# Kernel optimization log

Hardware: AMD Instinct MI355X
Metric: run time of the kernel (lower is better)

Reference implementation:

```python
import jax, jax.numpy as jnp
import numpy as np

N_ATOMS = 4096
N_EDGES = 131072
NUM_ELEMENTS = 100
NUM_BESSEL = 8
CUTOFF = 6.0
D_NODE = 64
D_MSG = 128
SH_DIM = 9            # l=0,1,2 -> 1+3+5
TP_IN = D_MSG * SH_DIM  # 1152
N_HEADS = 4
HEAD_DIM = D_MSG // N_HEADS


def setup_inputs() -> dict:
    key = jax.random.key(0)
    ks = jax.random.split(key, 20)
    def p(k, shape):
        return jax.random.normal(k, shape, dtype=jnp.float32) * 0.05
    z = lambda n: jnp.zeros((n,), jnp.float32)
    return {
        "atomic_numbers": jax.random.randint(ks[0], (N_ATOMS,), 0, NUM_ELEMENTS),
        "positions": jax.random.normal(ks[1], (N_ATOMS, 3), dtype=jnp.float32),
        "edge_index": jax.random.randint(ks[2], (2, N_EDGES), 0, N_ATOMS),
        "edge_vectors": jax.random.normal(ks[3], (N_EDGES, 3), dtype=jnp.float32),
        "edge_lengths": jax.random.uniform(ks[4], (N_EDGES,), dtype=jnp.float32, minval=0.5, maxval=5.5),
        "embed_table": p(ks[5], (NUM_ELEMENTS, D_NODE)),
        "W_r1": p(ks[6], (NUM_BESSEL, 64)), "b_r1": z(64),
        "W_r2": p(ks[7], (64, D_MSG)), "b_r2": z(D_MSG),
        "W_tp": p(ks[8], (TP_IN, D_MSG)), "b_tp": z(D_MSG),
        "W_m1": p(ks[9], (D_MSG, D_MSG)), "b_m1": z(D_MSG),
        "W_m2": p(ks[10], (D_MSG, D_MSG)), "b_m2": z(D_MSG),
        "W_qkv": p(ks[11], (D_MSG, 3 * D_MSG)), "b_qkv": z(3 * D_MSG),
        "W_ao": p(ks[12], (D_MSG, D_MSG)), "b_ao": z(D_MSG),
        "W_g": p(ks[13], (D_MSG, D_MSG)), "b_g": z(D_MSG),
        "W_o": p(ks[14], (D_MSG, D_MSG)), "b_o": z(D_MSG),
    }


def reference(atomic_numbers, positions, edge_index, edge_vectors, edge_lengths,
              embed_table, W_r1, b_r1, W_r2, b_r2, W_tp, b_tp,
              W_m1, b_m1, W_m2, b_m2, W_qkv, b_qkv, W_ao, b_ao,
              W_g, b_g, W_o, b_o):
    node_features = embed_table[atomic_numbers]  # [N, 64]

    # spherical harmonics (l = 0,1,2 -> 9 features), order as in source
    r = jnp.linalg.norm(edge_vectors, axis=-1, keepdims=True) + 1e-8
    u = edge_vectors / r
    x, y, z = u[:, 0], u[:, 1], u[:, 2]
    sh = jnp.stack([jnp.ones_like(x), y, z, x,
                    3.0 * z * z - 1.0, x * z, y * z, x * y, x * x - y * y], axis=-1)  # [E,9]

    # bessel RBF with cosine cutoff envelope
    freqs = jnp.arange(1, NUM_BESSEL + 1, dtype=jnp.float32) * (np.pi / CUTOFF)
    env = 0.5 * (jnp.cos(edge_lengths * (np.pi / CUTOFF)) + 1.0) * (edge_lengths < CUTOFF).astype(jnp.float32)
    rbf = jnp.sin(edge_lengths[:, None] * freqs) / edge_lengths[:, None] * env[:, None]  # [E,8]

    radial = jax.nn.silu(rbf @ W_r1 + b_r1)
    radial = jax.nn.silu(radial @ W_r2 + b_r2)  # [E,128]

    # per-edge outer product radial x sh, flattened per-l blocks then concatenated
    outer = radial[:, :, None] * sh[:, None, :]  # [E,128,9]
    E = outer.shape[0]
    edge_messages = jnp.concatenate([
        outer[:, :, 0:1].reshape(E, -1),   # l=0 -> 128
        outer[:, :, 1:4].reshape(E, -1),   # l=1 -> 384
        outer[:, :, 4:9].reshape(E, -1),   # l=2 -> 640
    ], axis=-1)                            # [E,1152]
    edge_messages = edge_messages @ W_tp + b_tp  # [E,128]

    # scatter-add aggregation onto destination nodes (index_add_)
    dst = edge_index[1]
    aggregated = jnp.zeros((node_features.shape[0], D_MSG), jnp.float32).at[dst].add(edge_messages)

    combined = jnp.concatenate([node_features, aggregated[:, :D_NODE]], axis=-1)  # [N,128]
    updated = jax.nn.silu(combined @ W_m1 + b_m1) @ W_m2 + b_m2                   # [N,128]

    # multi-head self-attention over all atoms (batch=1, seq=N)
    N = updated.shape[0]
    qkv = updated @ W_qkv + b_qkv
    q, k, v = jnp.split(qkv, 3, axis=-1)
    q = q.reshape(N, N_HEADS, HEAD_DIM)
    k = k.reshape(N, N_HEADS, HEAD_DIM)
    v = v.reshape(N, N_HEADS, HEAD_DIM)
    scores = jnp.einsum('nhd,mhd->hnm', q, k) / np.sqrt(HEAD_DIM).astype(np.float32)
    attn = jax.nn.softmax(scores, axis=-1)
    attended = jnp.einsum('hnm,mhd->nhd', attn, v).reshape(N, D_MSG)
    attended = attended @ W_ao + b_ao

    gate = jax.nn.sigmoid(updated @ W_g + b_g)
    out = gate * attended + (1.0 - gate) * updated
    return out @ W_o + b_o
```

## Files before the change

### kernel.cpp

```cpp
#include <hip/hip_runtime.h>
#include <hip/hip_bf16.h>
#include <math.h>

#define N_ATOMS 4096
#define N_EDGES 131072
#define PI6 0.52359877559829887308f

typedef __attribute__((ext_vector_type(4))) float f32x4;
typedef _Float16 h16;
typedef __attribute__((ext_vector_type(8))) _Float16 half8;

__device__ __forceinline__ float silu_f(float x) { return x / (1.0f + __expf(-x)); }

__device__ __forceinline__ unsigned pk2h(float lo, float hi) {
    h16 a = (h16)lo, b = (h16)hi;
    unsigned short ua, ub;
    __builtin_memcpy(&ua, &a, 2);
    __builtin_memcpy(&ub, &b, 2);
    return ((unsigned)ub << 16) | (unsigned)ua;
}

__global__ void wprep_kernel(const float* __restrict__ Wtp, float* __restrict__ Wsl)
{
    int idx = blockIdx.x * 256 + threadIdx.x;
    int o = idx & 63;
    int c = (idx >> 6) & 127;
    int s = idx >> 13;
    int row = (s == 0) ? c : (s < 4 ? 128 + c * 3 + (s - 1) : 512 + c * 5 + (s - 4));
    Wsl[idx] = Wtp[row * 128 + o];
}

__global__ void count_kernel(const int* __restrict__ eidx, int* __restrict__ deg)
{
    int e = blockIdx.x * 256 + threadIdx.x;
    atomicAdd(&deg[eidx[N_EDGES + e]], 1);
}

__global__ void scan_kernel(const int* __restrict__ deg, int* __restrict__ base,
                            int* __restrict__ cur)
{
    __shared__ int sums[1024];
    const int t = threadIdx.x;
    int v0 = deg[4*t], v1 = deg[4*t+1], v2 = deg[4*t+2], v3 = deg[4*t+3];
    int s = v0 + v1 + v2 + v3;
    sums[t] = s;
    __syncthreads();
    for (int off = 1; off < 1024; off <<= 1) {
        int x = (t >= off) ? sums[t - off] : 0;
        __syncthreads();
        sums[t] += x;
        __syncthreads();
    }
    int excl = (t > 0) ? sums[t - 1] : 0;
    base[4*t]   = excl;             cur[4*t]   = excl;
    base[4*t+1] = excl + v0;        cur[4*t+1] = excl + v0;
    base[4*t+2] = excl + v0 + v1;   cur[4*t+2] = excl + v0 + v1;
    base[4*t+3] = excl + v0 + v1 + v2; cur[4*t+3] = excl + v0 + v1 + v2;
}

__global__ void scatter_kernel(const int* __restrict__ eidx, int* __restrict__ cur,
                               int* __restrict__ sortedE)
{
    int e = blockIdx.x * 256 + threadIdx.x;
    int dst = eidx[N_EDGES + e];
    int p = atomicAdd(&cur[dst], 1);
    sortedE[p] = e;
}

__global__ __launch_bounds__(128) void agg_kernel(
    const float* __restrict__ evec, const float* __restrict__ elen,
    const int* __restrict__ sortedE, const int* __restrict__ base,
    const int* __restrict__ deg,
    const float* __restrict__ Wr1, const float* __restrict__ br1,
    const float* __restrict__ Wr2, const float* __restrict__ br2,
    const float* __restrict__ Wsl, const float* __restrict__ btp,
    float* __restrict__ agg)
{
    __shared__ float rbfL[4][8];
    __shared__ float shL[4][9];
    __shared__ __align__(16) float R1L[4][64];
    __shared__ __align__(16) float GL[1152];
    __shared__ __align__(16) float redL[8][64];

    const int t = threadIdx.x;
    const int dst = blockIdx.x;
    const int dg = deg[dst];
    const int bs = base[dst];

    float G[9] = {0.f,0.f,0.f,0.f,0.f,0.f,0.f,0.f,0.f};

    const int nch = (dg + 3) >> 2;
    for (int c = 0; c < nch; ++c) {
        __syncthreads();
        if (t < 32) {
            int el = t >> 3, f = t & 7;
            int ce = c * 4 + el;
            float v = 0.f;
            if (ce < dg) {
                int eid = sortedE[bs + ce];
                float len = elen[eid];
                float env = 0.5f * (cosf(len * PI6) + 1.0f) * (len < 6.0f ? 1.0f : 0.0f);
                v = sinf(len * ((float)(f + 1) * PI6)) * (env / len);
            }
            rbfL[el][f] = v;
        } else if (t < 36) {
            int el = t - 32;
            int ce = c * 4 + el;
            float s0=0,s1=0,s2=0,s3=0,s4=0,s5=0,s6=0,s7=0,s8=0;
            if (ce < dg) {
                int eid = sortedE[bs + ce];
                float vx = evec[eid*3], vy = evec[eid*3+1], vz = evec[eid*3+2];
                float r = sqrtf(vx*vx + vy*vy + vz*vz) + 1e-8f;
                float inv = 1.0f / r;
                float x = vx*inv, y = vy*inv, z = vz*inv;
                s0 = 1.0f; s1 = y; s2 = z; s3 = x;
                s4 = 3.0f*z*z - 1.0f; s5 = x*z; s6 = y*z; s7 = x*y; s8 = x*x - y*y;
            }
            shL[el][0]=s0; shL[el][1]=s1; shL[el][2]=s2; shL[el][3]=s3;
            shL[el][4]=s4; shL[el][5]=s5; shL[el][6]=s6; shL[el][7]=s7; shL[el][8]=s8;
        }
        __syncthreads();
        #pragma unroll
        for (int rep = 0; rep < 2; ++rep) {
            int tau = t + rep * 128;
            int el = tau >> 6, ko = tau & 63;
            float acc = br1[ko];
            #pragma unroll
            for (int f = 0; f < 8; ++f)
                acc = fmaf(rbfL[el][f], Wr1[f * 64 + ko], acc);
            R1L[el][ko] = silu_f(acc);
        }
        __syncthreads();
        float a0 = 0.f, a1 = 0.f, a2 = 0.f, a3 = 0.f;
        for (int j = 0; j < 64; ++j) {
            float w = Wr2[j * 128 + t];
            a0 = fmaf(R1L[0][j], w, a0);
            a1 = fmaf(R1L[1][j], w, a1);
            a2 = fmaf(R1L[2][j], w, a2);
            a3 = fmaf(R1L[3][j], w, a3);
        }
        float b2 = br2[t];
        int rem = dg - c * 4;
        if (rem > 0) { float r2 = silu_f(a0 + b2);
            #pragma unroll
            for (int s2 = 0; s2 < 9; ++s2) G[s2] = fmaf(shL[0][s2], r2, G[s2]); }
        if (rem > 1) { float r2 = silu_f(a1 + b2);
            #pragma unroll
            for (int s2 = 0; s2 < 9; ++s2) G[s2] = fmaf(shL[1][s2], r2, G[s2]); }
        if (rem > 2) { float r2 = silu_f(a2 + b2);
            #pragma unroll
            for (int s2 = 0; s2 < 9; ++s2) G[s2] = fmaf(shL[2][s2], r2, G[s2]); }
        if (rem > 3) { float r2 = silu_f(a3 + b2);
            #pragma unroll
            for (int s2 = 0; s2 < 9; ++s2) G[s2] = fmaf(shL[3][s2], r2, G[s2]); }
    }

    #pragma unroll
    for (int s2 = 0; s2 < 9; ++s2) GL[s2 * 128 + t] = G[s2];
    __syncthreads();

    const f32x4* Wsl4 = (const f32x4*)Wsl;
    const int og = (t & 15) * 4;
    const int q  = t >> 4;
    f32x4 acc4 = {0.f, 0.f, 0.f, 0.f};
    for (int i = 0; i < 144; ++i) {
        int f = q * 144 + i;
        float g = GL[f];
        f32x4 w = Wsl4[f * 16 + (t & 15)];
        acc4 = acc4 + w * g;
    }
    *(f32x4*)&redL[q][og] = acc4;
    __syncthreads();
    if (t < 64) {
        float sum = 0.f;
        #pragma unroll
        for (int q2 = 0; q2 < 8; ++q2) sum += redL[q2][t];
        agg[dst * 64 + t] = sum + (float)dg * btp[t];
    }
}

__global__ void combined_kernel(const int* __restrict__ an,
                                const float* __restrict__ emb,
                                const float* __restrict__ agg,
                                float* __restrict__ comb)
{
    int i = blockIdx.x * 256 + threadIdx.x;
    if (i < N_ATOMS * 64) {
        int n = i >> 6, d = i & 63;
        comb[n * 128 + d]      = emb[an[n] * 64 + d];
        comb[n * 128 + 64 + d] = agg[n * 64 + d];
    }
}

template <int ACT>
__global__ __launch_bounds__(256, 2) void gemm128(
    const float* __restrict__ A, const float* __restrict__ W,
    const float* __restrict__ bias, float* __restrict__ C, int N,
    const float* __restrict__ aux1, const float* __restrict__ aux2)
{
    __shared__ __align__(16) float AT[128][64];
    __shared__ __align__(16) float Ws[128][64];
    const int t  = threadIdx.x;
    const int M0 = blockIdx.x * 64;
    const int N0 = blockIdx.y * 64;

    for (int idx = t; idx < 64 * 128; idx += 256) {
        int m = idx >> 7, k = idx & 127;
        AT[k][m ^ ((k & 15) << 2)] = A[(M0 + m) * 128 + k];
    }
    for (int idx = t; idx < 128 * 64; idx += 256) {
        int k = idx >> 6, o = idx & 63;
        Ws[k][o] = W[k * N + N0 + o];
    }
    __syncthreads();

    const int m0 = (t & 15) * 4;
    const int o0 = (t >> 4) * 4;
    float acc[4][4] = {};
    #pragma unroll 2
    for (int k = 0; k < 128; ++k) {
        int xs = (k & 15) << 2;
        float4 a4 = *(const float4*)&AT[k][m0 ^ xs];
        float4 w4 = *(const float4*)&Ws[k][o0];
        float av[4] = {a4.x, a4.y, a4.z, a4.w};
        float wv[4] = {w4.x, w4.y, w4.z, w4.w};
        #pragma unroll
        for (int i = 0; i < 4; ++i)
            #pragma unroll
            for (int j = 0; j < 4; ++j)
                acc[i][j] = fmaf(av[i], wv[j], acc[i][j]);
    }

    #pragma unroll
    for (int i = 0; i < 4; ++i) {
        int m = M0 + m0 + i;
        #pragma unroll
        for (int j = 0; j < 4; ++j) {
            int o = N0 + o0 + j;
            float v = acc[i][j] + bias[o];
            if (ACT == 1) v = silu_f(v);
            if (ACT == 2) {
                float sg = 1.0f / (1.0f + __expf(-v));
                v = sg * aux1[m * 128 + o] + (1.0f - sg) * aux2[m * 128 + o];
            }
            C[m * N + o] = v;
        }
    }
}

__global__ void qkprep_kernel(const float* __restrict__ qkvf,
                              h16* __restrict__ Qh, h16* __restrict__ Kh)
{
    int i = blockIdx.x * 256 + threadIdx.x;
    int d = i & 31, n = (i >> 5) & 4095, h = i >> 17;
    Qh[(h * 4096 + n) * 32 + d] = (h16)(qkvf[n * 384 + h * 32 + d] * 0.17677669529663687f);
    Kh[(h * 4096 + n) * 32 + d] = (h16)(qkvf[n * 384 + 128 + h * 32 + d]);
}

__global__ void vtprep_kernel(const float* __restrict__ qkvf,
                              h16* __restrict__ VT)
{
    int i = blockIdx.x * 256 + threadIdx.x;
    int n = i & 4095, dh = i >> 12;
    VT[dh * 4096 + n] = (h16)qkvf[n * 384 + 256 + dh];
}

__global__ __launch_bounds__(256, 4) void attn_kernel(
    const h16* __restrict__ Qh, const h16* __restrict__ Kh,
    const h16* __restrict__ VT, float* __restrict__ attd)
{
    __shared__ float st[4][64][10];
    const int t = threadIdx.x, w = t >> 6, lane = t & 63;
    const int h = blockIdx.x >> 8, qt = blockIdx.x & 255;
    const int l15 = lane & 15, g = lane >> 4;

    const h16* Kb = Kh + (size_t)h * 4096 * 32;
    const h16* Vb = VT + (size_t)h * 32 * 4096;
    half8 Qf = *(const half8*)(Qh + ((size_t)(h * 4096 + qt * 16 + l15) * 32 + g * 8));

    float m = -1e30f, l = 0.0f;
    f32x4 O0 = {0.f,0.f,0.f,0.f}, O1 = {0.f,0.f,0.f,0.f};
    const f32x4 zf = {0.f,0.f,0.f,0.f};
    const int sAlane = l15 + ((g & 1) << 5);
    const bool hi = g >= 2;

    const int kvbase = w * 1024;
    for (int kt = 0; kt < 32; ++kt) {
        int kv0 = kvbase + kt * 32;
        half8 K0 = *(const half8*)(Kb + ((size_t)(kv0 + l15) * 32 + g * 8));
        half8 K1 = *(const half8*)(Kb + ((size_t)(kv0 + 16 + l15) * 32 + g * 8));
        f32x4 S0 = __builtin_amdgcn_mfma_f32_16x16x32_f16(K0, Qf, zf, 0, 0, 0);
        f32x4 S1 = __builtin_amdgcn_mfma_f32_16x16x32_f16(K1, Qf, zf, 0, 0, 0);

        float tmax = fmaxf(fmaxf(fmaxf(S0.x, S0.y), fmaxf(S0.z, S0.w)),
                           fmaxf(fmaxf(S1.x, S1.y), fmaxf(S1.z, S1.w)));
        tmax = fmaxf(tmax, __shfl_xor(tmax, 16));
        tmax = fmaxf(tmax, __shfl_xor(tmax, 32));
        float mn = fmaxf(m, tmax);
        float c = __expf(m - mn);
        m = mn;
        float p0[4], p1[4];
        float ts = 0.f;
        #pragma unroll
        for (int i = 0; i < 4; ++i) { p0[i] = __expf(S0[i] - mn); ts += p0[i]; }
        #pragma unroll
        for (int i = 0; i < 4; ++i) { p1[i] = __expf(S1[i] - mn); ts += p1[i]; }
        ts += __shfl_xor(ts, 16);
        ts += __shfl_xor(ts, 32);
        l = l * c + ts;
        #pragma unroll
        for (int i = 0; i < 4; ++i) { O0[i] *= c; O1[i] *= c; }

        unsigned A0 = pk2h(p0[0], p0[1]), A1 = pk2h(p0[2], p0[3]);
        unsigned A2 = pk2h(p1[0], p1[1]), A3 = pk2h(p1[2], p1[3]);
        unsigned t0 = (unsigned)__shfl((int)A0, sAlane);
        unsigned t1 = (unsigned)__shfl((int)A1, sAlane);
        unsigned t2 = (unsigned)__shfl((int)A2, sAlane);
        unsigned t3 = (unsigned)__shfl((int)A3, sAlane);
        unsigned u0 = (unsigned)__shfl((int)A0, sAlane + 16);
        unsigned u1 = (unsigned)__shfl((int)A1, sAlane + 16);
        unsigned u2 = (unsigned)__shfl((int)A2, sAlane + 16);
        unsigned u3 = (unsigned)__shfl((int)A3, sAlane + 16);
        union { unsigned u[4]; half8 v; } P;
        P.u[0] = hi ? t2 : t0;
        P.u[1] = hi ? t3 : t1;
        P.u[2] = hi ? u2 : u0;
        P.u[3] = hi ? u3 : u1;

        half8 V0 = *(const half8*)(Vb + ((size_t)l15 * 4096 + kv0 + g * 8));
        half8 V1 = *(const half8*)(Vb + ((size_t)(16 + l15) * 4096 + kv0 + g * 8));
        O0 = __builtin_amdgcn_mfma_f32_16x16x32_f16(V0, P.v, O0, 0, 0, 0);
        O1 = __builtin_amdgcn_mfma_f32_16x16x32_f16(V1, P.v, O1, 0, 0, 0);
    }

    #pragma unroll
    for (int i = 0; i < 4; ++i) { st[w][lane][i] = O0[i]; st[w][lane][4 + i] = O1[i]; }
    st[w][lane][8] = m;
    st[w][lane][9] = l;
    __syncthreads();

    if (w == 0) {
        float M = -1e30f;
        #pragma unroll
        for (int j = 0; j < 4; ++j) M = fmaxf(M, st[j][lane][8]);
        float L = 0.f, o0[4] = {}, o1[4] = {};
        #pragma unroll
        for (int j = 0; j < 4; ++j) {
            float f = __expf(st[j][lane][8] - M);
            L += st[j][lane][9] * f;
            #pragma unroll
            for (int i = 0; i < 4; ++i) {
                o0[i] = fmaf(st[j][lane][i], f, o0[i]);
                o1[i] = fmaf(st[j][lane][4 + i], f, o1[i]);
            }
        }
        float invL = 1.0f / L;
        int nq = qt * 16 + l15;
        #pragma unroll
        for (int i = 0; i < 4; ++i) {
            attd[nq * 128 + h * 32 + g * 4 + i]      = o0[i] * invL;
            attd[nq * 128 + h * 32 + 16 + g * 4 + i] = o1[i] * invL;
        }
    }
}

extern "C" void kernel_launch(void* const* d_in, const int* in_sizes, int n_in,
                              void* d_out, int out_size, void* d_ws, size_t ws_size,
                              hipStream_t stream) {
    const int*   an    = (const int*)d_in[0];
    const int*   eidx  = (const int*)d_in[2];
    const float* evec  = (const float*)d_in[3];
    const float* elen  = (const float*)d_in[4];
    const float* emb   = (const float*)d_in[5];
    const float* Wr1   = (const float*)d_in[6];
    const float* br1   = (const float*)d_in[7];
    const float* Wr2   = (const float*)d_in[8];
    const float* br2   = (const float*)d_in[9];
    const float* Wtp   = (const float*)d_in[10];
    const float* btp   = (const float*)d_in[11];
    const float* Wm1   = (const float*)d_in[12];
    const float* bm1   = (const float*)d_in[13];
    const float* Wm2   = (const float*)d_in[14];
    const float* bm2   = (const float*)d_in[15];
    const float* Wqkv  = (const float*)d_in[16];
    const float* bqkv  = (const float*)d_in[17];
    const float* Wao   = (const float*)d_in[18];
    const float* bao   = (const float*)d_in[19];
    const float* Wg    = (const float*)d_in[20];
    const float* bg    = (const float*)d_in[21];
    const float* Wo    = (const float*)d_in[22];
    const float* bo    = (const float*)d_in[23];

    float* ws    = (float*)d_ws;
    float* agg   = ws;
    float* comb  = agg  + N_ATOMS * 64;
    float* h1    = comb + N_ATOMS * 128;
    float* upd   = h1   + N_ATOMS * 128;
    float* qkvf  = upd  + N_ATOMS * 128;
    float* attd  = qkvf + N_ATOMS * 384;
    float* aob   = attd + N_ATOMS * 128;
    float* Wsl   = aob;
    float* outp  = comb;
    int* deg     = (int*)attd;
    int* base    = deg + 4096;
    int* cur     = base + 4096;
    int* sortedE = cur + 4096;
    h16* Qhb = (h16*)comb;
    h16* Khb = Qhb + 4 * 4096 * 32;
    h16* VTb = (h16*)h1;

    hipMemsetAsync(deg, 0, 4096 * sizeof(int), stream);

    count_kernel<<<512, 256, 0, stream>>>(eidx, deg);
    scan_kernel<<<1, 1024, 0, stream>>>(deg, base, cur);
    scatter_kernel<<<512, 256, 0, stream>>>(eidx, cur, sortedE);

    wprep_kernel<<<288, 256, 0, stream>>>(Wtp, Wsl);

    agg_kernel<<<N_ATOMS, 128, 0, stream>>>(
        evec, elen, sortedE, base, deg, Wr1, br1, Wr2, br2, Wsl, btp, agg);

    combined_kernel<<<(N_ATOMS * 64) / 256, 256, 0, stream>>>(an, emb, agg, comb);

    gemm128<1><<<dim3(64, 2), 256, 0, stream>>>(comb, Wm1, bm1, h1, 128, nullptr, nullptr);
    gemm128<0><<<dim3(64, 2), 256, 0, stream>>>(h1, Wm2, bm2, upd, 128, nullptr, nullptr);
    gemm128<0><<<dim3(64, 6), 256, 0, stream>>>(upd, Wqkv, bqkv, qkvf, 384, nullptr, nullptr);

    qkprep_kernel<<<2048, 256, 0, stream>>>(qkvf, Qhb, Khb);
    vtprep_kernel<<<2048, 256, 0, stream>>>(qkvf, VTb);

    attn_kernel<<<1024, 256, 0, stream>>>(Qhb, Khb, VTb, attd);

    gemm128<0><<<dim3(64, 2), 256, 0, stream>>>(attd, Wao, bao, aob, 128, nullptr, nullptr);
    gemm128<2><<<dim3(64, 2), 256, 0, stream>>>(upd, Wg, bg, outp, 128, aob, upd);
    gemm128<0><<<dim3(64, 2), 256, 0, stream>>>(outp, Wo, bo, (float*)d_out, 128, nullptr, nullptr);
}
```

Baseline: 298.7 us.

## Process 16 edges per chunk and move G·W_tp projection into batched GEMM

The per-node aggregation kernel now handles 16 edges per iteration instead of 4, computing the radial MLP with vectorized register tiles so each loaded Wr2 value is reused across more edges. The per-node 1152x64 projection is taken out of that kernel. The intermediate G features are written to a workspace buffer and multiplied in a separate tiled GEMM kernel that reuses W_tp across 32 nodes per block. The work runs in two halves of 2048 nodes so that G fits in the reused workspace. This adds global round trips for G and extra launches, and nodes with fewer than 16 edges waste part of each chunk.

```diff
diff --git a/kernel.cpp b/kernel.cpp
--- a/kernel.cpp
+++ b/kernel.cpp
@@ -70,42 +70,43 @@
 __global__ __launch_bounds__(128) void agg_kernel(
     const float* __restrict__ evec, const float* __restrict__ elen,
     const int* __restrict__ sortedE, const int* __restrict__ base,
-    const int* __restrict__ deg,
+    const int* __restrict__ deg, int aoff,
     const float* __restrict__ Wr1, const float* __restrict__ br1,
     const float* __restrict__ Wr2, const float* __restrict__ br2,
-    const float* __restrict__ Wsl, const float* __restrict__ btp,
-    float* __restrict__ agg)
-{
-    __shared__ float rbfL[4][8];
-    __shared__ float shL[4][9];
-    __shared__ __align__(16) float R1L[4][64];
-    __shared__ __align__(16) float GL[1152];
-    __shared__ __align__(16) float redL[8][64];
+    float* __restrict__ Gm)
+{
+    __shared__ __align__(16) float rbfL[16][8];
+    __shared__ float shL[16][9];
+    __shared__ __align__(16) float R1L[64][16];
+    __shared__ __align__(16) float R2L[16][128];
 
     const int t = threadIdx.x;
-    const int dst = blockIdx.x;
+    const int dst = aoff + blockIdx.x;
     const int dg = deg[dst];
     const int bs = base[dst];
 
+    const int el8 = t >> 3, f8 = t & 7;
+    const int e4 = t >> 5, c4 = t & 31;
+    const int elR = t & 15, koR = t >> 4;
+
     float G[9] = {0.f,0.f,0.f,0.f,0.f,0.f,0.f,0.f,0.f};
 
-    const int nch = (dg + 3) >> 2;
+    const int nch = (dg + 15) >> 4;
     for (int c = 0; c < nch; ++c) {
         __syncthreads();
-        if (t < 32) {
-            int el = t >> 3, f = t & 7;
-            int ce = c * 4 + el;
+        {
+            int ce = c * 16 + el8;
             float v = 0.f;
             if (ce < dg) {
                 int eid = sortedE[bs + ce];
                 float len = elen[eid];
                 float env = 0.5f * (cosf(len * PI6) + 1.0f) * (len < 6.0f ? 1.0f : 0.0f);
-                v = sinf(len * ((float)(f + 1) * PI6)) * (env / len);
-            }
-            rbfL[el][f] = v;
-        } else if (t < 36) {
-            int el = t - 32;
-            int ce = c * 4 + el;
+                v = sinf(len * ((float)(f8 + 1) * PI6)) * (env / len);
+            }
+            rbfL[el8][f8] = v;
+        }
+        if (t < 16) {
+            int ce = c * 16 + t;
             float s0=0,s1=0,s2=0,s3=0,s4=0,s5=0,s6=0,s7=0,s8=0;
             if (ce < dg) {
                 int eid = sortedE[bs + ce];
@@ -116,66 +117,115 @@
                 s0 = 1.0f; s1 = y; s2 = z; s3 = x;
                 s4 = 3.0f*z*z - 1.0f; s5 = x*z; s6 = y*z; s7 = x*y; s8 = x*x - y*y;
             }
-            shL[el][0]=s0; shL[el][1]=s1; shL[el][2]=s2; shL[el][3]=s3;
-            shL[el][4]=s4; shL[el][5]=s5; shL[el][6]=s6; shL[el][7]=s7; shL[el][8]=s8;
-        }
-        __syncthreads();
-        #pragma unroll
-        for (int rep = 0; rep < 2; ++rep) {
-            int tau = t + rep * 128;
-            int el = tau >> 6, ko = tau & 63;
-            float acc = br1[ko];
+            shL[t][0]=s0; shL[t][1]=s1; shL[t][2]=s2; shL[t][3]=s3;
+            shL[t][4]=s4; shL[t][5]=s5; shL[t][6]=s6; shL[t][7]=s7; shL[t][8]=s8;
+        }
+        __syncthreads();
+        {
+            f32x4 rb0 = *(const f32x4*)&rbfL[elR][0];
+            f32x4 rb1 = *(const f32x4*)&rbfL[elR][4];
             #pragma unroll
-            for (int f = 0; f < 8; ++f)
-                acc = fmaf(rbfL[el][f], Wr1[f * 64 + ko], acc);
-            R1L[el][ko] = silu_f(acc);
-        }
-        __syncthreads();
-        float a0 = 0.f, a1 = 0.f, a2 = 0.f, a3 = 0.f;
-        for (int j = 0; j < 64; ++j) {
-            float w = Wr2[j * 128 + t];
-            a0 = fmaf(R1L[0][j], w, a0);
-            a1 = fmaf(R1L[1][j], w, a1);
-            a2 = fmaf(R1L[2][j], w, a2);
-            a3 = fmaf(R1L[3][j], w, a3);
-        }
-        float b2 = br2[t];
-        int rem = dg - c * 4;
-        if (rem > 0) { float r2 = silu_f(a0 + b2);
+            for (int rep = 0; rep < 8; ++rep) {
+                int ko = koR + rep * 8;
+                float acc = br1[ko];
+                acc = fmaf(rb0.x, Wr1[0*64 + ko], acc);
+                acc = fmaf(rb0.y, Wr1[1*64 + ko], acc);
+                acc = fmaf(rb0.z, Wr1[2*64 + ko], acc);
+                acc = fmaf(rb0.w, Wr1[3*64 + ko], acc);
+                acc = fmaf(rb1.x, Wr1[4*64 + ko], acc);
+                acc = fmaf(rb1.y, Wr1[5*64 + ko], acc);
+                acc = fmaf(rb1.z, Wr1[6*64 + ko], acc);
+                acc = fmaf(rb1.w, Wr1[7*64 + ko], acc);
+                R1L[ko][elR] = silu_f(acc);
+            }
+        }
+        __syncthreads();
+        {
+            f32x4 a0 = {0.f,0.f,0.f,0.f}, a1 = a0, a2 = a0, a3 = a0;
+            const float* Wp = Wr2 + c4 * 4;
+            #pragma unroll 4
+            for (int j = 0; j < 64; ++j) {
+                f32x4 r = *(const f32x4*)&R1L[j][e4 * 4];
+                f32x4 w = *(const f32x4*)&Wp[j * 128];
+                a0 += w * r.x;
+                a1 += w * r.y;
+                a2 += w * r.z;
+                a3 += w * r.w;
+            }
+            f32x4 b2 = *(const f32x4*)&br2[c4 * 4];
+            a0 += b2; a1 += b2; a2 += b2; a3 += b2;
+            f32x4 o0, o1, o2, o3;
             #pragma unroll
-            for (int s2 = 0; s2 < 9; ++s2) G[s2] = fmaf(shL[0][s2], r2, G[s2]); }
-        if (rem > 1) { float r2 = silu_f(a1 + b2);
+            for (int q = 0; q < 4; ++q) {
+                o0[q] = silu_f(a0[q]); o1[q] = silu_f(a1[q]);
+                o2[q] = silu_f(a2[q]); o3[q] = silu_f(a3[q]);
+            }
+            *(f32x4*)&R2L[e4*4 + 0][c4*4] = o0;
+            *(f32x4*)&R2L[e4*4 + 1][c4*4] = o1;
+            *(f32x4*)&R2L[e4*4 + 2][c4*4] = o2;
+            *(f32x4*)&R2L[e4*4 + 3][c4*4] = o3;
+        }
+        __syncthreads();
+        {
+            int rem = dg - c * 16; if (rem > 16) rem = 16;
+            for (int el = 0; el < rem; ++el) {
+                float r2 = R2L[el][t];
+                #pragma unroll
+                for (int s = 0; s < 9; ++s) G[s] = fmaf(shL[el][s], r2, G[s]);
+            }
+        }
+    }
+
+    #pragma unroll
+    for (int s = 0; s < 9; ++s) Gm[blockIdx.x * 1152 + s * 128 + t] = G[s];
+}
+
+__global__ __launch_bounds__(256, 2) void gemm_gw(
+    const float* __restrict__ Gm, const float* __restrict__ Wsl,
+    const int* __restrict__ deg, const float* __restrict__ btp, int aoff,
+    float* __restrict__ agg)
+{
+    __shared__ __align__(16) float AT[128][32];
+    __shared__ __align__(16) float Ws[128][64];
+    const int t  = threadIdx.x;
+    const int M0 = blockIdx.x * 32;
+    const int m0 = (t & 15) * 2;
+    const int o0 = (t >> 4) * 4;
+    float acc[2][4] = {};
+
+    for (int kk = 0; kk < 9; ++kk) {
+        __syncthreads();
+        for (int idx = t; idx < 32 * 128; idx += 256) {
+            int m = idx >> 7, k = idx & 127;
+            AT[k][m ^ ((k & 7) << 2)] = Gm[(M0 + m) * 1152 + kk * 128 + k];
+        }
+        for (int idx = t; idx < 128 * 64; idx += 256) {
+            int k = idx >> 6, o = idx & 63;
+            Ws[k][o] = Wsl[(kk * 128 + k) * 64 + o];
+        }
+        __syncthreads();
+        #pragma unroll 2
+        for (int k = 0; k < 128; ++k) {
+            int xs = (k & 7) << 2;
+            float2 a2 = *(const float2*)&AT[k][m0 ^ xs];
+            float4 w4 = *(const float4*)&Ws[k][o0];
+            float av[2] = {a2.x, a2.y};
+            float wv[4] = {w4.x, w4.y, w4.z, w4.w};
             #pragma unroll
-            for (int s2 = 0; s2 < 9; ++s2) G[s2] = fmaf(shL[1][s2], r2, G[s2]); }
-        if (rem > 2) { float r2 = silu_f(a2 + b2);
-            #pragma unroll
-            for (int s2 = 0; s2 < 9; ++s2) G[s2] = fmaf(shL[2][s2], r2, G[s2]); }
-        if (rem > 3) { float r2 = silu_f(a3 + b2);
-            #pragma unroll
-            for (int s2 = 0; s2 < 9; ++s2) G[s2] = fmaf(shL[3][s2], r2, G[s2]); }
+            for (int i = 0; i < 2; ++i)
+                #pragma unroll
+                for (int j = 0; j < 4; ++j)
+                    acc[i][j] = fmaf(av[i], wv[j], acc[i][j]);
+        }
     }
 
     #pragma unroll
-    for (int s2 = 0; s2 < 9; ++s2) GL[s2 * 128 + t] = G[s2];
-    __syncthreads();
-
-    const f32x4* Wsl4 = (const f32x4*)Wsl;
-    const int og = (t & 15) * 4;
-    const int q  = t >> 4;
-    f32x4 acc4 = {0.f, 0.f, 0.f, 0.f};
-    for (int i = 0; i < 144; ++i) {
-        int f = q * 144 + i;
-        float g = GL[f];
-        f32x4 w = Wsl4[f * 16 + (t & 15)];
-        acc4 = acc4 + w * g;
-    }
-    *(f32x4*)&redL[q][og] = acc4;
-    __syncthreads();
-    if (t < 64) {
-        float sum = 0.f;
-        #pragma unroll
-        for (int q2 = 0; q2 < 8; ++q2) sum += redL[q2][t];
-        agg[dst * 64 + t] = sum + (float)dg * btp[t];
+    for (int i = 0; i < 2; ++i) {
+        int m = M0 + m0 + i;
+        float dgm = (float)deg[aoff + m];
+        #pragma unroll
+        for (int j = 0; j < 4; ++j)
+            agg[(aoff + m) * 64 + o0 + j] = acc[i][j] + dgm * btp[o0 + j];
     }
 }
 
@@ -400,6 +450,7 @@
     float* attd  = qkvf + N_ATOMS * 384;
     float* aob   = attd + N_ATOMS * 128;
     float* Wsl   = aob;
+    float* Gm    = comb;
     float* outp  = comb;
     int* deg     = (int*)attd;
     int* base    = deg + 4096;
@@ -417,8 +468,12 @@
 
     wprep_kernel<<<288, 256, 0, stream>>>(Wtp, Wsl);
 
-    agg_kernel<<<N_ATOMS, 128, 0, stream>>>(
-        evec, elen, sortedE, base, deg, Wr1, br1, Wr2, br2, Wsl, btp, agg);
+    agg_kernel<<<2048, 128, 0, stream>>>(
+        evec, elen, sortedE, base, deg, 0, Wr1, br1, Wr2, br2, Gm);
+    gemm_gw<<<64, 256, 0, stream>>>(Gm, Wsl, deg, btp, 0, agg);
+    agg_kernel<<<2048, 128, 0, stream>>>(
+        evec, elen, sortedE, base, deg, 2048, Wr1, br1, Wr2, br2, Gm);
+    gemm_gw<<<64, 256, 0, stream>>>(Gm, Wsl, deg, btp, 2048, agg);
 
     combined_kernel<<<(N_ATOMS * 64) / 256, 256, 0, stream>>>(an, emb, agg, comb);
 
```

After: 409.3 us. +37.0%, slower.
